# Performance work log

Measured on AMD Instinct MI355X. Metric: run time of the kernel, lower is better.

## Reference

```python
import jax, jax.numpy as jnp
import numpy as np

BOS_IDX = 1


def setup_inputs() -> dict:
    key = jax.random.key(0)
    ks = jax.random.split(key, 12)
    B, T, S, H, L, V = 16, 128, 64, 512, 2, 32000
    s = 0.05
    return {
        "encoder_outputs": jax.random.normal(ks[0], (B, S, H), jnp.float32),
        "encoder_h": jax.random.normal(ks[1], (L, B, H), jnp.float32) * s,
        "encoder_c": jax.random.normal(ks[2], (L, B, H), jnp.float32) * s,
        "target_tensor": jax.random.randint(ks[3], (B, T), 0, V),
        "embedding": jax.random.normal(ks[4], (V, H), jnp.float32) * s,
        "W_ih": jax.random.normal(ks[5], (L, 4 * H, H), jnp.float32) * s,
        "W_hh": jax.random.normal(ks[6], (L, 4 * H, H), jnp.float32) * s,
        "b_ih": jax.random.normal(ks[7], (L, 4 * H), jnp.float32) * s,
        "b_hh": jax.random.normal(ks[8], (L, 4 * H), jnp.float32) * s,
        "W_out": jax.random.normal(ks[9], (V, H), jnp.float32) * s,
        "b_out": jax.random.normal(ks[10], (V,), jnp.float32) * s,
    }


def reference(encoder_outputs, encoder_h, encoder_c, target_tensor,
              embedding, W_ih, W_hh, b_ih, b_hh, W_out, b_out):
    B, T = target_tensor.shape
    L = W_ih.shape[0]
    # Teacher-forced inputs: BOS then target[:, :-1]
    tokens = jnp.concatenate(
        [jnp.full((B, 1), BOS_IDX, dtype=target_tensor.dtype),
         target_tensor[:, :-1]], axis=1)  # [B, T]
    x = jax.nn.relu(embedding[tokens])  # [B, T, H]
    # The original loop resets (h, c) to encoder_states at EVERY step, so all
    # T single-step LSTM cells are independent -> vectorize over T.
    h_last, c_last = [], []
    for l in range(L):
        h0 = encoder_h[l]  # [B, H]
        c0 = encoder_c[l][:, None, :]  # [B, 1, H]
        gates = (jnp.einsum('bth,gh->btg', x, W_ih[l]) + b_ih[l]
                 + (jnp.einsum('bh,gh->bg', h0, W_hh[l]) + b_hh[l])[:, None, :])
        i, f, g, o = jnp.split(gates, 4, axis=-1)  # torch gate order i,f,g,o
        c = jax.nn.sigmoid(f) * c0 + jax.nn.sigmoid(i) * jnp.tanh(g)
        h = jax.nn.sigmoid(o) * jnp.tanh(c)  # [B, T, H]
        h_last.append(h[:, -1, :])
        c_last.append(c[:, -1, :])
        x = h  # input to next layer (dropout=0 / eval)
    logits = jnp.einsum('bth,vh->btv', x, W_out) + b_out  # [B, T, V]
    return logits, (jnp.stack(h_last), jnp.stack(c_last))
```

## Files before the change

### kernel.cpp

```cpp
#include <hip/hip_runtime.h>
#include <hip/hip_bf16.h>

typedef __bf16 bf16_t;
typedef __bf16 bf16x8 __attribute__((ext_vector_type(8)));
typedef __bf16 bf16x4 __attribute__((ext_vector_type(4)));
typedef float f32x4 __attribute__((ext_vector_type(4)));

#define B_ 16
#define T_ 128
#define H_ 512
#define L_ 2
#define V_ 32000
#define G_ 2048
#define M_ 2048

#define BM 128
#define BN 128
#define BK 32

__global__ __launch_bounds__(256) void cvt_bf16(const float* __restrict__ in,
                                                bf16_t* __restrict__ out) {
    int idx = blockIdx.x * 256 + threadIdx.x;
    float4 v = ((const float4*)in)[idx];
    bf16x4 o;
    o[0] = (bf16_t)v.x; o[1] = (bf16_t)v.y; o[2] = (bf16_t)v.z; o[3] = (bf16_t)v.w;
    ((bf16x4*)out)[idx] = o;
}

__global__ __launch_bounds__(256) void embed_relu(const float* __restrict__ emb,
                                                  const int* __restrict__ target,
                                                  bf16_t* __restrict__ x) {
    int idx = blockIdx.x * 256 + threadIdx.x;
    int m  = idx >> 7;
    int h4 = (idx & 127) << 2;
    int b = m >> 7, t = m & 127;
    int tok = (t == 0) ? 1 : target[b * T_ + t - 1];
    float4 v = *(const float4*)(emb + (size_t)tok * H_ + h4);
    bf16x4 o;
    o[0] = (bf16_t)fmaxf(v.x, 0.f);
    o[1] = (bf16_t)fmaxf(v.y, 0.f);
    o[2] = (bf16_t)fmaxf(v.z, 0.f);
    o[3] = (bf16_t)fmaxf(v.w, 0.f);
    *(bf16x4*)(x + (size_t)m * H_ + h4) = o;
}

__global__ __launch_bounds__(256) void hproj_kernel(const float* __restrict__ enc_h,
                                                    const float* __restrict__ W_hh,
                                                    const float* __restrict__ b_ih,
                                                    const float* __restrict__ b_hh,
                                                    float* __restrict__ biasall) {
    int idx = blockIdx.x * 256 + threadIdx.x;
    int b = idx & 15;
    int g = (idx >> 4) & (G_ - 1);
    int l = idx >> 15;
    const float* hrow = enc_h + ((size_t)l * B_ + b) * H_;
    const float* wrow = W_hh + ((size_t)l * G_ + g) * H_;
    float acc = b_ih[l * G_ + g] + b_hh[l * G_ + g];
    #pragma unroll 4
    for (int k = 0; k < H_; k += 4) {
        float4 hv = *(const float4*)(hrow + k);
        float4 wv = *(const float4*)(wrow + k);
        acc += hv.x * wv.x + hv.y * wv.y + hv.z * wv.z + hv.w * wv.w;
    }
    biasall[((size_t)l * B_ + b) * G_ + g] = acc;
}

__global__ __launch_bounds__(256) void gemm_bt(const bf16_t* __restrict__ A,
                                               const bf16_t* __restrict__ B,
                                               float* __restrict__ C,
                                               const float* __restrict__ bias,
                                               int M, int N, int K, int bias_mode) {
    __shared__ __align__(16) bf16_t As[BM * BK];
    __shared__ __align__(16) bf16_t Bs[BN * BK];

    const int tid  = threadIdx.x;
    const int lane = tid & 63;
    const int wave = tid >> 6;
    const int wm = wave >> 1, wn = wave & 1;
    const int quad = lane >> 4;
    const int r16  = lane & 15;

    const int tileM = blockIdx.x * BM;
    const int tileN = blockIdx.y * BN;

    const int srow = lane >> 2;
    const int scol = (lane & 3) * 8;

    f32x4 acc[4][4];
    #pragma unroll
    for (int i = 0; i < 4; i++)
        #pragma unroll
        for (int j = 0; j < 4; j++) acc[i][j] = (f32x4){0.f, 0.f, 0.f, 0.f};

    const int nk = K / BK;
    for (int kt = 0; kt < nk; ++kt) {
        const int k0 = kt * BK;
        #pragma unroll
        for (int j = 0; j < 2; ++j) {
            const int r0 = j * 64 + wave * 16;
            const bf16_t* ga = A + (size_t)(tileM + r0 + srow) * K + k0 + scol;
            const bf16_t* gb = B + (size_t)(tileN + r0 + srow) * K + k0 + scol;
            __builtin_amdgcn_global_load_lds(
                (const __attribute__((address_space(1))) void*)ga,
                (__attribute__((address_space(3))) void*)(As + r0 * BK), 16, 0, 0);
            __builtin_amdgcn_global_load_lds(
                (const __attribute__((address_space(1))) void*)gb,
                (__attribute__((address_space(3))) void*)(Bs + r0 * BK), 16, 0, 0);
        }
        __syncthreads();

        bf16x8 af[4], bfr[4];
        #pragma unroll
        for (int mi = 0; mi < 4; mi++)
            af[mi] = *(const bf16x8*)(As + (wm * 64 + mi * 16 + r16) * BK + quad * 8);
        #pragma unroll
        for (int ni = 0; ni < 4; ni++)
            bfr[ni] = *(const bf16x8*)(Bs + (wn * 64 + ni * 16 + r16) * BK + quad * 8);
        #pragma unroll
        for (int mi = 0; mi < 4; mi++)
            #pragma unroll
            for (int ni = 0; ni < 4; ni++)
                acc[mi][ni] = __builtin_amdgcn_mfma_f32_16x16x32_bf16(
                    af[mi], bfr[ni], acc[mi][ni], 0, 0, 0);
        __syncthreads();
    }

    const float* brow = bias_mode ? (bias + (size_t)blockIdx.x * N) : bias;
    #pragma unroll
    for (int mi = 0; mi < 4; mi++) {
        #pragma unroll
        for (int ni = 0; ni < 4; ni++) {
            const int col = tileN + wn * 64 + ni * 16 + r16;
            const float bv = brow[col];
            #pragma unroll
            for (int rr = 0; rr < 4; rr++) {
                const int row = tileM + wm * 64 + mi * 16 + quad * 4 + rr;
                C[(size_t)row * N + col] = acc[mi][ni][rr] + bv;
            }
        }
    }
}

__device__ __forceinline__ float sigf(float x) { return 1.f / (1.f + __expf(-x)); }
__device__ __forceinline__ float tanhf_(float x) { return 2.f / (1.f + __expf(-2.f * x)) - 1.f; }

__global__ __launch_bounds__(256) void lstm_cell(const float* __restrict__ gates,
                                                 const float* __restrict__ enc_c,
                                                 bf16_t* __restrict__ x,
                                                 float* __restrict__ out_h,
                                                 float* __restrict__ out_c,
                                                 int l) {
    int idx = blockIdx.x * 256 + threadIdx.x;
    int m  = idx >> 9;
    int hh = idx & (H_ - 1);
    int b = m >> 7, t = m & 127;
    const float* grow = gates + (size_t)m * G_;
    float gi = grow[hh];
    float gf = grow[H_ + hh];
    float gg = grow[2 * H_ + hh];
    float go = grow[3 * H_ + hh];
    float c0 = enc_c[((size_t)l * B_ + b) * H_ + hh];
    float c = sigf(gf) * c0 + sigf(gi) * tanhf_(gg);
    float h = sigf(go) * tanhf_(c);
    x[idx] = (bf16_t)h;
    if (t == T_ - 1) {
        out_h[((size_t)l * B_ + b) * H_ + hh] = h;
        out_c[((size_t)l * B_ + b) * H_ + hh] = c;
    }
}

extern "C" void kernel_launch(void* const* d_in, const int* in_sizes, int n_in,
                              void* d_out, int out_size, void* d_ws, size_t ws_size,
                              hipStream_t stream) {
    const float* enc_h  = (const float*)d_in[1];
    const float* enc_c  = (const float*)d_in[2];
    const int*   target = (const int*)d_in[3];
    const float* emb    = (const float*)d_in[4];
    const float* W_ih   = (const float*)d_in[5];
    const float* W_hh   = (const float*)d_in[6];
    const float* b_ih   = (const float*)d_in[7];
    const float* b_hh   = (const float*)d_in[8];
    const float* W_out  = (const float*)d_in[9];
    const float* b_out  = (const float*)d_in[10];
    float* out = (float*)d_out;

    char* w = (char*)d_ws;
    bf16_t* x       = (bf16_t*)(w);
    bf16_t* wih_b   = (bf16_t*)(w + 2097152);
    bf16_t* wout_b  = (bf16_t*)(w + 6291456);
    float*  gates   = (float*)(w + 39059456);
    float*  biasall = (float*)(w + 55836672);

    float* out_h = out + (size_t)M_ * V_;
    float* out_c = out_h + (size_t)L_ * B_ * H_;

    cvt_bf16<<<(L_ * G_ * H_) / 1024, 256, 0, stream>>>(W_ih, wih_b);
    cvt_bf16<<<(V_ * H_) / 1024, 256, 0, stream>>>(W_out, wout_b);
    embed_relu<<<(M_ * H_ / 4) / 256, 256, 0, stream>>>(emb, target, x);
    hproj_kernel<<<(L_ * G_ * B_) / 256, 256, 0, stream>>>(enc_h, W_hh, b_ih, b_hh, biasall);

    for (int l = 0; l < L_; ++l) {
        dim3 gg(M_ / BM, G_ / BN);
        gemm_bt<<<gg, 256, 0, stream>>>(x, wih_b + (size_t)l * G_ * H_, gates,
                                        biasall + (size_t)l * B_ * G_, M_, G_, H_, 1);
        lstm_cell<<<(M_ * H_) / 256, 256, 0, stream>>>(gates, enc_c, x, out_h, out_c, l);
    }

    dim3 gl(M_ / BM, V_ / BN);
    gemm_bt<<<gl, 256, 0, stream>>>(x, wout_b, out, b_out, M_, V_, H_, 0);
}
```

Measured before the change: 523.3 us.

## Fuse LSTM cell into gate GEMM epilogue and merge prep kernels

Reorders W_ih rows and the recurrent bias so that each 16-column group holds the i,f,g,o gates for the same hidden units. This lets the gate GEMM epilogue compute the LSTM cell directly and write bf16 h, with no fp32 gates buffer round-trip and no separate cell kernel. All preprocessing (weight conversion, embedding, hidden projection) is merged into one launch. It also adds an XCD-aware block remapping and nontemporal stores for the large logits output. The cost is a more complex epilogue, with transcendental math done per accumulator inside the GEMM.

```diff
diff --git a/kernel.cpp b/kernel.cpp
--- a/kernel.cpp
+++ b/kernel.cpp
@@ -18,58 +18,86 @@
 #define BN 128
 #define BK 32
 
-__global__ __launch_bounds__(256) void cvt_bf16(const float* __restrict__ in,
-                                                bf16_t* __restrict__ out) {
-    int idx = blockIdx.x * 256 + threadIdx.x;
-    float4 v = ((const float4*)in)[idx];
-    bf16x4 o;
-    o[0] = (bf16_t)v.x; o[1] = (bf16_t)v.y; o[2] = (bf16_t)v.z; o[3] = (bf16_t)v.w;
-    ((bf16x4*)out)[idx] = o;
-}
-
-__global__ __launch_bounds__(256) void embed_relu(const float* __restrict__ emb,
-                                                  const int* __restrict__ target,
-                                                  bf16_t* __restrict__ x) {
-    int idx = blockIdx.x * 256 + threadIdx.x;
-    int m  = idx >> 7;
-    int h4 = (idx & 127) << 2;
-    int b = m >> 7, t = m & 127;
-    int tok = (t == 0) ? 1 : target[b * T_ + t - 1];
-    float4 v = *(const float4*)(emb + (size_t)tok * H_ + h4);
-    bf16x4 o;
-    o[0] = (bf16_t)fmaxf(v.x, 0.f);
-    o[1] = (bf16_t)fmaxf(v.y, 0.f);
-    o[2] = (bf16_t)fmaxf(v.z, 0.f);
-    o[3] = (bf16_t)fmaxf(v.w, 0.f);
-    *(bf16x4*)(x + (size_t)m * H_ + h4) = o;
-}
-
-__global__ __launch_bounds__(256) void hproj_kernel(const float* __restrict__ enc_h,
-                                                    const float* __restrict__ W_hh,
-                                                    const float* __restrict__ b_ih,
-                                                    const float* __restrict__ b_hh,
-                                                    float* __restrict__ biasall) {
-    int idx = blockIdx.x * 256 + threadIdx.x;
-    int b = idx & 15;
-    int g = (idx >> 4) & (G_ - 1);
-    int l = idx >> 15;
-    const float* hrow = enc_h + ((size_t)l * B_ + b) * H_;
-    const float* wrow = W_hh + ((size_t)l * G_ + g) * H_;
-    float acc = b_ih[l * G_ + g] + b_hh[l * G_ + g];
-    #pragma unroll 4
-    for (int k = 0; k < H_; k += 4) {
-        float4 hv = *(const float4*)(hrow + k);
-        float4 wv = *(const float4*)(wrow + k);
-        acc += hv.x * wv.x + hv.y * wv.y + hv.z * wv.z + hv.w * wv.w;
+__device__ __forceinline__ float sigf(float x) { return 1.f / (1.f + __expf(-x)); }
+__device__ __forceinline__ float tanhf_(float x) { return 2.f / (1.f + __expf(-2.f * x)) - 1.f; }
+
+
+__global__ __launch_bounds__(256) void prep(const float* __restrict__ emb,
+                                            const int* __restrict__ target,
+                                            const float* __restrict__ enc_h,
+                                            const float* __restrict__ W_ih,
+                                            const float* __restrict__ W_hh,
+                                            const float* __restrict__ b_ih,
+                                            const float* __restrict__ b_hh,
+                                            const float* __restrict__ W_out,
+                                            bf16_t* __restrict__ x,
+                                            bf16_t* __restrict__ wih_b,
+                                            bf16_t* __restrict__ wout_b,
+                                            float* __restrict__ biasall) {
+    const int blk = blockIdx.x;
+    const int tid = threadIdx.x;
+    if (blk < 256) {
+        int idx = blk * 256 + tid;
+        int b = idx & 15;
+        int c = (idx >> 4) & (G_ - 1);
+        int l = idx >> 15;
+        int gate = (c >> 4) & 3;
+        int h = ((c >> 6) << 4) | (c & 15);
+        int r = gate * H_ + h;
+        const float* hrow = enc_h + ((size_t)l * B_ + b) * H_;
+        const float* wrow = W_hh + ((size_t)l * G_ + r) * H_;
+        float acc = b_ih[l * G_ + r] + b_hh[l * G_ + r];
+        #pragma unroll 4
+        for (int k = 0; k < H_; k += 4) {
+            float4 hv = *(const float4*)(hrow + k);
+            float4 wv = *(const float4*)(wrow + k);
+            acc += hv.x * wv.x + hv.y * wv.y + hv.z * wv.z + hv.w * wv.w;
+        }
+        biasall[((size_t)l * B_ + b) * G_ + c] = acc;
+    } else if (blk < 2304) {
+        int idx = (blk - 256) * 256 + tid;
+        int k4 = idx & 127;
+        int c  = (idx >> 7) & (G_ - 1);
+        int l  = idx >> 18;
+        int gate = (c >> 4) & 3;
+        int h = ((c >> 6) << 4) | (c & 15);
+        int r = gate * H_ + h;
+        float4 v = *(const float4*)(W_ih + ((size_t)l * G_ + r) * H_ + k4 * 4);
+        bf16x4 o;
+        o[0] = (bf16_t)v.x; o[1] = (bf16_t)v.y; o[2] = (bf16_t)v.z; o[3] = (bf16_t)v.w;
+        *(bf16x4*)(wih_b + ((size_t)l * G_ + c) * H_ + k4 * 4) = o;
+    } else if (blk < 3328) {
+        int idx = (blk - 2304) * 256 + tid;
+        int m  = idx >> 7;
+        int h4 = (idx & 127) << 2;
+        int b = m >> 7, t = m & 127;
+        int tok = (t == 0) ? 1 : target[b * T_ + t - 1];
+        float4 v = *(const float4*)(emb + (size_t)tok * H_ + h4);
+        bf16x4 o;
+        o[0] = (bf16_t)fmaxf(v.x, 0.f);
+        o[1] = (bf16_t)fmaxf(v.y, 0.f);
+        o[2] = (bf16_t)fmaxf(v.z, 0.f);
+        o[3] = (bf16_t)fmaxf(v.w, 0.f);
+        *(bf16x4*)(x + (size_t)m * H_ + h4) = o;
+    } else {
+        int idx = (blk - 3328) * 256 + tid;
+        float4 v = ((const float4*)W_out)[idx];
+        bf16x4 o;
+        o[0] = (bf16_t)v.x; o[1] = (bf16_t)v.y; o[2] = (bf16_t)v.z; o[3] = (bf16_t)v.w;
+        ((bf16x4*)wout_b)[idx] = o;
     }
-    biasall[((size_t)l * B_ + b) * G_ + g] = acc;
 }
 
 __global__ __launch_bounds__(256) void gemm_bt(const bf16_t* __restrict__ A,
                                                const bf16_t* __restrict__ B,
                                                float* __restrict__ C,
                                                const float* __restrict__ bias,
-                                               int M, int N, int K, int bias_mode) {
+                                               int M, int N, int K, int mode,
+                                               const float* __restrict__ enc_c,
+                                               bf16_t* __restrict__ xout,
+                                               float* __restrict__ out_h,
+                                               float* __restrict__ out_c,
+                                               int l) {
     __shared__ __align__(16) bf16_t As[BM * BK];
     __shared__ __align__(16) bf16_t Bs[BN * BK];
 
@@ -80,8 +108,13 @@
     const int quad = lane >> 4;
     const int r16  = lane & 15;
 
-    const int tileM = blockIdx.x * BM;
-    const int tileN = blockIdx.y * BN;
+    const int nwg = gridDim.x;
+    const int q = nwg >> 3;
+    const int wg = (blockIdx.x & 7) * q + (blockIdx.x >> 3);
+    const int bx = wg & 15;
+    const int by = wg >> 4;
+    const int tileM = bx * BM;
+    const int tileN = by * BN;
 
     const int srow = lane >> 2;
     const int scol = (lane & 3) * 8;
@@ -125,47 +158,48 @@
         __syncthreads();
     }
 
-    const float* brow = bias_mode ? (bias + (size_t)blockIdx.x * N) : bias;
-    #pragma unroll
-    for (int mi = 0; mi < 4; mi++) {
-        #pragma unroll
-        for (int ni = 0; ni < 4; ni++) {
-            const int col = tileN + wn * 64 + ni * 16 + r16;
-            const float bv = brow[col];
+    if (mode == 0) {
+        #pragma unroll
+        for (int mi = 0; mi < 4; mi++) {
+            #pragma unroll
+            for (int ni = 0; ni < 4; ni++) {
+                const int col = tileN + wn * 64 + ni * 16 + r16;
+                const float bv = bias[col];
+                #pragma unroll
+                for (int rr = 0; rr < 4; rr++) {
+                    const int row = tileM + wm * 64 + mi * 16 + quad * 4 + rr;
+                    __builtin_nontemporal_store(acc[mi][ni][rr] + bv,
+                                                &C[(size_t)row * N + col]);
+                }
+            }
+        }
+    } else {
+        const int b = bx;
+        const float* brow = bias + (size_t)b * G_;
+        float bv[4];
+        #pragma unroll
+        for (int g = 0; g < 4; g++)
+            bv[g] = brow[tileN + wn * 64 + g * 16 + r16];
+        const int h = (2 * by + wn) * 16 + r16;
+        const float c0 = enc_c[((size_t)l * B_ + b) * H_ + h];
+        #pragma unroll
+        for (int mi = 0; mi < 4; mi++) {
             #pragma unroll
             for (int rr = 0; rr < 4; rr++) {
-                const int row = tileM + wm * 64 + mi * 16 + quad * 4 + rr;
-                C[(size_t)row * N + col] = acc[mi][ni][rr] + bv;
+                const int t = wm * 64 + mi * 16 + quad * 4 + rr;
+                const float gi = acc[mi][0][rr] + bv[0];
+                const float gf = acc[mi][1][rr] + bv[1];
+                const float gg = acc[mi][2][rr] + bv[2];
+                const float go = acc[mi][3][rr] + bv[3];
+                const float c = sigf(gf) * c0 + sigf(gi) * tanhf_(gg);
+                const float hv = sigf(go) * tanhf_(c);
+                xout[(size_t)(b * T_ + t) * H_ + h] = (bf16_t)hv;
+                if (t == T_ - 1) {
+                    out_h[((size_t)l * B_ + b) * H_ + h] = hv;
+                    out_c[((size_t)l * B_ + b) * H_ + h] = c;
+                }
             }
         }
-    }
-}
-
-__device__ __forceinline__ float sigf(float x) { return 1.f / (1.f + __expf(-x)); }
-__device__ __forceinline__ float tanhf_(float x) { return 2.f / (1.f + __expf(-2.f * x)) - 1.f; }
-
-__global__ __launch_bounds__(256) void lstm_cell(const float* __restrict__ gates,
-                                                 const float* __restrict__ enc_c,
-                                                 bf16_t* __restrict__ x,
-                                                 float* __restrict__ out_h,
-                                                 float* __restrict__ out_c,
-                                                 int l) {
-    int idx = blockIdx.x * 256 + threadIdx.x;
-    int m  = idx >> 9;
-    int hh = idx & (H_ - 1);
-    int b = m >> 7, t = m & 127;
-    const float* grow = gates + (size_t)m * G_;
-    float gi = grow[hh];
-    float gf = grow[H_ + hh];
-    float gg = grow[2 * H_ + hh];
-    float go = grow[3 * H_ + hh];
-    float c0 = enc_c[((size_t)l * B_ + b) * H_ + hh];
-    float c = sigf(gf) * c0 + sigf(gi) * tanhf_(gg);
-    float h = sigf(go) * tanhf_(c);
-    x[idx] = (bf16_t)h;
-    if (t == T_ - 1) {
-        out_h[((size_t)l * B_ + b) * H_ + hh] = h;
-        out_c[((size_t)l * B_ + b) * H_ + hh] = c;
     }
 }
 
@@ -188,24 +222,23 @@
     bf16_t* x       = (bf16_t*)(w);
     bf16_t* wih_b   = (bf16_t*)(w + 2097152);
     bf16_t* wout_b  = (bf16_t*)(w + 6291456);
-    float*  gates   = (float*)(w + 39059456);
+    bf16_t* x2      = (bf16_t*)(w + 39059456);
     float*  biasall = (float*)(w + 55836672);
 
     float* out_h = out + (size_t)M_ * V_;
     float* out_c = out_h + (size_t)L_ * B_ * H_;
 
-    cvt_bf16<<<(L_ * G_ * H_) / 1024, 256, 0, stream>>>(W_ih, wih_b);
-    cvt_bf16<<<(V_ * H_) / 1024, 256, 0, stream>>>(W_out, wout_b);
-    embed_relu<<<(M_ * H_ / 4) / 256, 256, 0, stream>>>(emb, target, x);
-    hproj_kernel<<<(L_ * G_ * B_) / 256, 256, 0, stream>>>(enc_h, W_hh, b_ih, b_hh, biasall);
-
-    for (int l = 0; l < L_; ++l) {
-        dim3 gg(M_ / BM, G_ / BN);
-        gemm_bt<<<gg, 256, 0, stream>>>(x, wih_b + (size_t)l * G_ * H_, gates,
-                                        biasall + (size_t)l * B_ * G_, M_, G_, H_, 1);
-        lstm_cell<<<(M_ * H_) / 256, 256, 0, stream>>>(gates, enc_c, x, out_h, out_c, l);
-    }
-
-    dim3 gl(M_ / BM, V_ / BN);
-    gemm_bt<<<gl, 256, 0, stream>>>(x, wout_b, out, b_out, M_, V_, H_, 0);
+    prep<<<19328, 256, 0, stream>>>(emb, target, enc_h, W_ih, W_hh, b_ih, b_hh,
+                                    W_out, x, wih_b, wout_b, biasall);
+
+    gemm_bt<<<(M_ / BM) * (G_ / BN), 256, 0, stream>>>(
+        x, wih_b, (float*)x2, biasall, M_, G_, H_, 1,
+        enc_c, x2, out_h, out_c, 0);
+    gemm_bt<<<(M_ / BM) * (G_ / BN), 256, 0, stream>>>(
+        x2, wih_b + (size_t)G_ * H_, (float*)x, biasall + (size_t)B_ * G_,
+        M_, G_, H_, 1, enc_c, x, out_h, out_c, 1);
+
+    gemm_bt<<<(M_ / BM) * (V_ / BN), 256, 0, stream>>>(
+        x, wout_b, out, b_out, M_, V_, H_, 0,
+        nullptr, nullptr, nullptr, nullptr, 0);
 }
```

Result: faster. 497.9 us (-4.9%).
